# Optimization experiments

Measured on AMD Instinct MI355X. Metric: run time of the kernel, lower is better.

The kernel has to match this reference:

```python
import jax, jax.numpy as jnp
import numpy as np


def setup_inputs() -> dict:
    key = jax.random.key(0)
    k1, k2 = jax.random.split(key)
    B, C, H, W, F = 32, 256, 64, 64, 256
    inputs = jax.random.normal(k1, (B, C, H, W), dtype=jnp.float32)
    biases = jax.random.normal(k2, (1, 1, C, F), dtype=jnp.float32)
    return {"inputs": inputs, "biases": biases}


def _mix_weights(biases):
    # UnitSphereInit.get_log_prob: unit-sphere parameterization of a
    # probability vector over input channels: p_cf = b_cf^2 / sum_c b_cf^2.
    # The original computes log(p) and later exponentiates inside logsumexp;
    # we keep p directly (same math, fewer transcendentals).
    sq = biases * biases                      # (1,1,C,F)
    p = sq / jnp.sum(sq, axis=2, keepdims=True)
    return p.reshape(biases.shape[2], biases.shape[3])  # (C, F)


def reference(inputs, biases):
    # out[b,f,h,w] = logsumexp_c( x[b,c,h,w] + log p[c,f] )
    #             = m[b,h,w] + log( sum_c exp(x - m) * p[c,f] )
    # p <= 1 so the exp is safe; the channel reduction over all filters
    # fuses into one GEMM (single pass over the input, all filters at once).
    p = _mix_weights(biases)                          # (C, F)
    m = jnp.max(inputs, axis=1, keepdims=True)        # (B,1,H,W)
    e = jnp.exp(inputs - m)                           # (B,C,H,W)
    s = jnp.einsum('bchw,cf->bfhw', e, p)             # (B,F,H,W)
    return m + jnp.log(s)
```

## Files before the change

### kernel.cpp

```cpp
#include <hip/hip_runtime.h>
#include <stdint.h>

#define C_DIM 256
#define F_DIM 256
#define HW    4096
#define TILE  64

typedef __attribute__((ext_vector_type(8))) short   bf16x8;
typedef __attribute__((ext_vector_type(4))) float   floatx4;

__device__ __forceinline__ unsigned short f32_to_bf16(float f) {
    union { float f; unsigned int u; } v; v.f = f;
    unsigned int u = v.u;
    return (unsigned short)((u + 0x7FFFu + ((u >> 16) & 1u)) >> 16);
}

__global__ void prep_kernel(const float* __restrict__ b,
                            unsigned short* __restrict__ apack) {
    __shared__ float part[16][17];
    __shared__ float inv_s[16];
    const int t     = threadIdx.x;
    const int ftile = blockIdx.x;
    const int f0    = ftile * 16;

    const int fl = t & 15;
    const int cg = t >> 4;
    float s = 0.f;
#pragma unroll
    for (int k = 0; k < 16; ++k) {
        float v = b[(cg + 16 * k) * F_DIM + f0 + fl];
        s += v * v;
    }
    part[cg][fl] = s;
    __syncthreads();
    if (t < 16) {
        float acc = 0.f;
#pragma unroll
        for (int g = 0; g < 16; ++g) acc += part[g][t];
        inv_s[t] = 1.0f / acc;
    }
    __syncthreads();

#pragma unroll
    for (int e = t; e < 512; e += 256) {
        const int kiter = e >> 6;
        const int lane  = e & 63;
        const int f     = f0 + (lane & 15);
        const int c0    = kiter * 32 + ((lane >> 4) << 3);
        const float inv = inv_s[lane & 15];
        bf16x8 v;
#pragma unroll
        for (int i = 0; i < 8; ++i) {
            float w = b[(c0 + i) * F_DIM + f];
            v[i] = (short)f32_to_bf16(w * w * inv);
        }
        *(bf16x8*)(apack + ((size_t)(ftile * 8 + kiter) * 64 + lane) * 8) = v;
    }
}

#define ETPAD 264

__global__ __launch_bounds__(256, 4)
void mixture_kernel(const float* __restrict__ x,
                    const unsigned short* __restrict__ apack,
                    float* __restrict__ out) {
    __shared__ __align__(16) unsigned short eT[TILE][ETPAD];

    const int t     = threadIdx.x;
    const int batch = blockIdx.x >> 6;
    const int hw0   = (blockIdx.x & 63) << 6;

    const int j = t & 63;
    const int s = t >> 6;

    const float* xp = x + ((size_t)batch * C_DIM + (size_t)s * 64) * HW + hw0 + j;
#pragma unroll 2
    for (int cc = 0; cc < 8; ++cc) {
        float xv[8];
#pragma unroll
        for (int i = 0; i < 8; ++i) xv[i] = xp[(size_t)(cc * 8 + i) * HW];
        bf16x8 v;
#pragma unroll
        for (int i = 0; i < 8; ++i) v[i] = (short)f32_to_bf16(__expf(xv[i]));
        *(bf16x8*)&eT[j][(s << 6) + (cc << 3)] = v;
    }
    __syncthreads();

    const int wv  = s;
    const int llo = t & 15;
    const int lhi = (t & 63) >> 4;
    const int lane = t & 63;

    floatx4 acc[4][4];
#pragma unroll
    for (int a = 0; a < 4; ++a)
#pragma unroll
        for (int jt = 0; jt < 4; ++jt)
            acc[a][jt] = (floatx4){0.f, 0.f, 0.f, 0.f};

    const bf16x8* ap = (const bf16x8*)apack;

#pragma unroll
    for (int k = 0; k < 8; ++k) {
        bf16x8 bfrag[4];
#pragma unroll
        for (int jt = 0; jt < 4; ++jt)
            bfrag[jt] = *(const bf16x8*)&eT[jt * 16 + llo][k * 32 + lhi * 8];
#pragma unroll
        for (int a = 0; a < 4; ++a) {
            bf16x8 afrag = ap[((4 * wv + a) * 8 + k) * 64 + lane];
#pragma unroll
            for (int jt = 0; jt < 4; ++jt)
                acc[a][jt] = __builtin_amdgcn_mfma_f32_16x16x32_bf16(
                    afrag, bfrag[jt], acc[a][jt], 0, 0, 0);
        }
    }

    float* ob = out + (size_t)batch * F_DIM * HW + hw0;
#pragma unroll
    for (int a = 0; a < 4; ++a) {
        const int fbase = wv * 64 + a * 16 + lhi * 4;
#pragma unroll
        for (int r = 0; r < 4; ++r) {
            float* orow = ob + (size_t)(fbase + r) * HW;
#pragma unroll
            for (int jt = 0; jt < 4; ++jt)
                orow[jt * 16 + llo] = __logf(acc[a][jt][r]);
        }
    }
}

extern "C" void kernel_launch(void* const* d_in, const int* in_sizes, int n_in,
                              void* d_out, int out_size, void* d_ws, size_t ws_size,
                              hipStream_t stream) {
    const float* x      = (const float*)d_in[0];
    const float* biases = (const float*)d_in[1];
    float* out = (float*)d_out;

    unsigned short* apack = (unsigned short*)d_ws;

    prep_kernel<<<16, 256, 0, stream>>>(biases, apack);
    mixture_kernel<<<2048, 256, 0, stream>>>(x, apack, out);
}
```

Measured before the change: 249.2 us.

## Double-buffer input chunks via async global-to-LDS loads with wider tiles

Restructures the mixture kernel to stream the channel dimension in 32-channel chunks. Each chunk is loaded with global_load_lds into a double-buffered LDS staging area while the previous chunk is exponentiated, converted to bf16 and fed to MFMA. The tile widens to 128 pixels and the block grows to 512 threads, with each wave owning 32 filters. The aim is to overlap HBM reads with compute instead of loading the whole tile up front. In exchange it adds per-chunk barriers and relies on hand-written waitcnt counts that must match the number of outstanding loads.

Result: faster. 242.4 us (-2.7%).

```diff
diff --git a/kernel.cpp b/kernel.cpp
--- a/kernel.cpp
+++ b/kernel.cpp
@@ -1,10 +1,12 @@
 #include <hip/hip_runtime.h>
 #include <stdint.h>
 
-#define C_DIM 256
-#define F_DIM 256
-#define HW    4096
-#define TILE  64
+#define C_DIM  256
+#define F_DIM  256
+#define HW     4096
+#define TW     128
+#define NCHUNK 8
+#define ETP    40
 
 typedef __attribute__((ext_vector_type(8))) short   bf16x8;
 typedef __attribute__((ext_vector_type(4))) float   floatx4;
@@ -13,6 +15,12 @@
     union { float f; unsigned int u; } v; v.f = f;
     unsigned int u = v.u;
     return (unsigned short)((u + 0x7FFFu + ((u >> 16) & 1u)) >> 16);
+}
+
+__device__ __forceinline__ void async_load16(const float* g, float* l) {
+    __builtin_amdgcn_global_load_lds(
+        (const __attribute__((address_space(1))) void*)g,
+        (__attribute__((address_space(3))) void*)l, 16, 0, 0);
 }
 
 __global__ void prep_kernel(const float* __restrict__ b,
@@ -58,73 +66,92 @@
     }
 }
 
-#define ETPAD 264
-
-__global__ __launch_bounds__(256, 4)
+__global__ __launch_bounds__(512, 4)
 void mixture_kernel(const float* __restrict__ x,
                     const unsigned short* __restrict__ apack,
                     float* __restrict__ out) {
-    __shared__ __align__(16) unsigned short eT[TILE][ETPAD];
+    __shared__ __align__(16) float          sbuf[2][32][TW];
+    __shared__ __align__(16) unsigned short et[2][TW][ETP];
 
     const int t     = threadIdx.x;
-    const int batch = blockIdx.x >> 6;
-    const int hw0   = (blockIdx.x & 63) << 6;
+    const int wv    = t >> 6;
+    const int lane  = t & 63;
+    const int batch = blockIdx.x >> 5;
+    const int hw0   = (blockIdx.x & 31) * TW;
 
-    const int j = t & 63;
-    const int s = t >> 6;
+    const float* xb = x + (size_t)batch * C_DIM * HW + hw0;
 
-    const float* xp = x + ((size_t)batch * C_DIM + (size_t)s * 64) * HW + hw0 + j;
-#pragma unroll 2
-    for (int cc = 0; cc < 8; ++cc) {
-        float xv[8];
+#define DMA_CHUNK(ck, buf)                                                      \
+    {                                                                           \
+        _Pragma("unroll")                                                       \
+        for (int r = 0; r < 2; ++r) {                                           \
+            const int rr = 4 * wv + 2 * r;                                      \
+            const float* g = xb + (size_t)((ck) * 32 + rr + (lane >> 5)) * HW   \
+                                + (lane & 31) * 4;                              \
+            async_load16(g, &sbuf[buf][rr][0]);                                 \
+        }                                                                       \
+    }
+
+    const int llo = lane & 15;
+    const int lhi = lane >> 4;
+    const int j   = t & 127;
+    const int cg  = t >> 7;
+
+    floatx4 acc[2][8];
 #pragma unroll
-        for (int i = 0; i < 8; ++i) xv[i] = xp[(size_t)(cc * 8 + i) * HW];
-        bf16x8 v;
+    for (int a = 0; a < 2; ++a)
 #pragma unroll
-        for (int i = 0; i < 8; ++i) v[i] = (short)f32_to_bf16(__expf(xv[i]));
-        *(bf16x8*)&eT[j][(s << 6) + (cc << 3)] = v;
-    }
-    __syncthreads();
-
-    const int wv  = s;
-    const int llo = t & 15;
-    const int lhi = (t & 63) >> 4;
-    const int lane = t & 63;
-
-    floatx4 acc[4][4];
-#pragma unroll
-    for (int a = 0; a < 4; ++a)
-#pragma unroll
-        for (int jt = 0; jt < 4; ++jt)
+        for (int jt = 0; jt < 8; ++jt)
             acc[a][jt] = (floatx4){0.f, 0.f, 0.f, 0.f};
 
     const bf16x8* ap = (const bf16x8*)apack;
 
+    DMA_CHUNK(0, 0);
+
 #pragma unroll
-    for (int k = 0; k < 8; ++k) {
-        bf16x8 bfrag[4];
+    for (int i = 0; i < NCHUNK; ++i) {
+        const int b = i & 1;
+
+        bf16x8 afrag0 = ap[((2 * wv + 0) * 8 + i) * 64 + lane];
+        bf16x8 afrag1 = ap[((2 * wv + 1) * 8 + i) * 64 + lane];
+
+        if (i < NCHUNK - 1) {
+            DMA_CHUNK(i + 1, b ^ 1);
+            asm volatile("s_waitcnt vmcnt(2)\n\ts_barrier" ::: "memory");
+        } else {
+            asm volatile("s_waitcnt vmcnt(0)\n\ts_barrier" ::: "memory");
+        }
+
+        {
+            float xv[8];
 #pragma unroll
-        for (int jt = 0; jt < 4; ++jt)
-            bfrag[jt] = *(const bf16x8*)&eT[jt * 16 + llo][k * 32 + lhi * 8];
+            for (int q = 0; q < 8; ++q) xv[q] = sbuf[b][cg * 8 + q][j];
+            bf16x8 v;
 #pragma unroll
-        for (int a = 0; a < 4; ++a) {
-            bf16x8 afrag = ap[((4 * wv + a) * 8 + k) * 64 + lane];
+            for (int q = 0; q < 8; ++q) v[q] = (short)f32_to_bf16(__expf(xv[q]));
+            *(bf16x8*)&et[b][j][cg * 8] = v;
+        }
+        asm volatile("s_waitcnt lgkmcnt(0)\n\ts_barrier" ::: "memory");
+
 #pragma unroll
-            for (int jt = 0; jt < 4; ++jt)
-                acc[a][jt] = __builtin_amdgcn_mfma_f32_16x16x32_bf16(
-                    afrag, bfrag[jt], acc[a][jt], 0, 0, 0);
+        for (int jt = 0; jt < 8; ++jt) {
+            bf16x8 bfrag = *(const bf16x8*)&et[b][jt * 16 + llo][lhi * 8];
+            acc[0][jt] = __builtin_amdgcn_mfma_f32_16x16x32_bf16(
+                afrag0, bfrag, acc[0][jt], 0, 0, 0);
+            acc[1][jt] = __builtin_amdgcn_mfma_f32_16x16x32_bf16(
+                afrag1, bfrag, acc[1][jt], 0, 0, 0);
         }
     }
 
     float* ob = out + (size_t)batch * F_DIM * HW + hw0;
 #pragma unroll
-    for (int a = 0; a < 4; ++a) {
-        const int fbase = wv * 64 + a * 16 + lhi * 4;
+    for (int a = 0; a < 2; ++a) {
+        const int fbase = 32 * wv + 16 * a + lhi * 4;
 #pragma unroll
         for (int r = 0; r < 4; ++r) {
             float* orow = ob + (size_t)(fbase + r) * HW;
 #pragma unroll
-            for (int jt = 0; jt < 4; ++jt)
+            for (int jt = 0; jt < 8; ++jt)
                 orow[jt * 16 + llo] = __logf(acc[a][jt][r]);
         }
     }
@@ -140,5 +167,5 @@
     unsigned short* apack = (unsigned short*)d_ws;
 
     prep_kernel<<<16, 256, 0, stream>>>(biases, apack);
-    mixture_kernel<<<2048, 256, 0, stream>>>(x, apack, out);
+    mixture_kernel<<<1024, 512, 0, stream>>>(x, apack, out);
 }
```
